# Kernel optimization log

Hardware: AMD Instinct MI355X
Metric: run time of the kernel (lower is better)

## Reference

```python
import jax, jax.numpy as jnp
import numpy as np

E = 21   # numParticipants (experts)
D = 128  # input features (hardcoded Linear(128,16))
H = 16   # hidden
N = 262144  # rows


def setup_inputs() -> dict:
    key = jax.random.key(0)
    ks = jax.random.split(key, 6)
    x = jax.random.normal(ks[0], (N, D), dtype=jnp.float32)
    sid = jax.random.randint(ks[1], (N,), 0, E)
    s1 = 1.0 / np.sqrt(D)
    W1 = jax.random.uniform(ks[2], (E, D, H), jnp.float32, -s1, s1)
    b1 = jax.random.uniform(ks[3], (E, H), jnp.float32, -s1, s1)
    s2 = 1.0 / np.sqrt(H)
    W2 = jax.random.uniform(ks[4], (E, H), jnp.float32, -s2, s2)  # Linear(16,1) weight, squeezed
    b2 = jax.random.uniform(ks[5], (E,), jnp.float32, -s2, s2)
    return {"x": x, "sid": sid, "W1": W1, "b1": b1, "W2": W2, "b2": b2}


def reference(x, sid, W1, b1, W2, b2):
    # Per-row expert MLP: h = relu(x @ W1[sid] + b1[sid]); y = relu(h . W2[sid] + b2[sid]).
    # Dropout(0.5) is identity in eval mode. Vectorized routing: compute first layer for
    # all 21 tiny experts ([N,E,H] ~ 350MB), then select the routed expert per row.
    h_all = jax.nn.relu(jnp.einsum('nd,edh->neh', x, W1) + b1[None, :, :])  # [N,E,H]
    h = jnp.take_along_axis(h_all, sid[:, None, None], axis=1)[:, 0, :]      # [N,H]
    y = jax.nn.relu(jnp.einsum('nh,nh->n', h, W2[sid]) + b2[sid])            # [N]
    return y[:, None]  # [N,1]
```

## Files before the change

kernel.cpp:

```cpp
#include <hip/hip_runtime.h>
#include <stdint.h>

#define N_ROWS 262144
#define DIM    128
#define HID    16
#define NEXP   21
#define NSEG   (N_ROWS / 64 + NEXP)
#define NBLK1  256
#define RPB    (N_ROWS / NBLK1)
#define RPT    (RPB / 256)

#define PADB     1040
#define WAVE_LDS (8 * PADB)
#define BLK_LDS  (4 * WAVE_LDS)

__global__ __launch_bounds__(256) void k_hist(const int* __restrict__ sid,
                                              int* __restrict__ counts,
                                              int* __restrict__ blockBase) {
    __shared__ int lh[NEXP];
    int t = threadIdx.x;
    if (t < NEXP) lh[t] = 0;
    __syncthreads();
    int base = blockIdx.x * RPB + t;
#pragma unroll
    for (int r = 0; r < RPT; r++) {
        atomicAdd(&lh[sid[base + r * 256]], 1);
    }
    __syncthreads();
    if (t < NEXP) blockBase[blockIdx.x * NEXP + t] = atomicAdd(&counts[t], lh[t]);
}

__global__ __launch_bounds__(256) void k_scatter(const int* __restrict__ sid,
                                                 const int* __restrict__ counts,
                                                 const int* __restrict__ blockBase,
                                                 int* __restrict__ buckets) {
    __shared__ int sbase[NEXP];
    __shared__ int lcur[NEXP];
    int t = threadIdx.x;
    if (t == 0) {
        int acc = 0;
        for (int e = 0; e < NEXP; e++) {
            sbase[e] = acc + blockBase[blockIdx.x * NEXP + e];
            acc += ((counts[e] + 63) >> 6) << 6;
        }
    }
    if (t < NEXP) lcur[t] = 0;
    __syncthreads();
    int base = blockIdx.x * RPB + t;
#pragma unroll
    for (int r = 0; r < RPT; r++) {
        int row = base + r * 256;
        int e = sid[row];
        int lp = atomicAdd(&lcur[e], 1);
        buckets[sbase[e] + lp] = row | (e << 24);
    }
}

typedef __attribute__((address_space(1))) const uint32_t gu32;
typedef __attribute__((address_space(3))) uint32_t lu32;

__device__ __forceinline__ void stage16(const float* gp, char* lp) {
    __builtin_amdgcn_global_load_lds((gu32*)(uintptr_t)gp,
                                     (lu32*)(uintptr_t)lp, 16, 0, 0);
}

__device__ __forceinline__ float bcast(float v, int lane) {
    return __uint_as_float(__builtin_amdgcn_readlane(__float_as_uint(v), lane));
}

__global__ __launch_bounds__(256, 4) void k_main4(const float* __restrict__ x,
                                                  const float* __restrict__ W1,
                                                  const float* __restrict__ b1,
                                                  const float* __restrict__ W2,
                                                  const float* __restrict__ b2,
                                                  const int* __restrict__ buckets,
                                                  float* __restrict__ out) {
    extern __shared__ char smem[];
    const int seg = blockIdx.x * 4 + (threadIdx.x >> 6);
    if (seg >= NSEG) return;
    const int lane = threadIdx.x & 63;
    char* waveLds = smem + (threadIdx.x >> 6) * WAVE_LDS;

    int ent = buckets[seg * 64 + lane];
    if (__ballot(ent >= 0) == 0ULL) return;
    const int e = __builtin_amdgcn_readfirstlane(ent) >> 24;
    const int row = ent & 0x00FFFFFF;
    const int vrow = (ent >= 0) ? row : 0;

    int rg[8];
#pragma unroll
    for (int g = 0; g < 8; g++) rg[g] = __shfl(vrow, g * 8 + (lane >> 3), 64);
    const int c8 = lane & 7;

    const float* __restrict__ w1 = W1 + e * (DIM * HID);
    float h[HID];
#pragma unroll
    for (int j = 0; j < HID; j++) h[j] = b1[e * HID + j];

    const char* rb = waveLds + (lane >> 3) * PADB + (lane & 7) * 128;

#pragma unroll 1
    for (int q = 0; q < 4; q++) {
        __builtin_amdgcn_s_waitcnt(0);
#pragma unroll
        for (int g = 0; g < 8; g++) {
            const float* gp = x + (size_t)rg[g] * DIM + q * 32 + c8 * 4;
            stage16(gp, waveLds + g * PADB + lane * 16);
        }
        const float* __restrict__ w1q = w1 + q * 512;
        float wq[8];
#pragma unroll
        for (int m = 0; m < 8; m++) wq[m] = w1q[m * 64 + lane];
        __builtin_amdgcn_s_waitcnt(0);
#pragma unroll
        for (int m = 0; m < 8; m++) {
            const float4 xv = *(const float4*)(rb + m * 16);
            const float xc[4] = {xv.x, xv.y, xv.z, xv.w};
#pragma unroll
            for (int c = 0; c < 4; c++) {
#pragma unroll
                for (int j = 0; j < HID; j++)
                    h[j] = fmaf(xc[c], bcast(wq[m], c * 16 + j), h[j]);
            }
        }
    }

    float acc = b2[e];
#pragma unroll
    for (int j = 0; j < HID; j++) acc = fmaf(fmaxf(h[j], 0.0f), W2[e * HID + j], acc);
    if (ent >= 0) out[row] = fmaxf(acc, 0.0f);
}

__global__ __launch_bounds__(256) void k_naive(const float* __restrict__ x,
                                               const int* __restrict__ sid,
                                               const float* __restrict__ W1,
                                               const float* __restrict__ b1,
                                               const float* __restrict__ W2,
                                               const float* __restrict__ b2,
                                               float* __restrict__ out) {
    int row = blockIdx.x * 256 + threadIdx.x;
    if (row >= N_ROWS) return;
    int e = sid[row];
    const float* w1 = W1 + e * (DIM * HID);
    const float* xr = x + (size_t)row * DIM;
    float h[HID];
#pragma unroll
    for (int j = 0; j < HID; j++) h[j] = b1[e * HID + j];
    for (int k = 0; k < DIM; k++) {
        float xk = xr[k];
#pragma unroll
        for (int j = 0; j < HID; j++) h[j] = fmaf(xk, w1[k * HID + j], h[j]);
    }
    float acc = b2[e];
#pragma unroll
    for (int j = 0; j < HID; j++) acc = fmaf(fmaxf(h[j], 0.0f), W2[e * HID + j], acc);
    out[row] = fmaxf(acc, 0.0f);
}

extern "C" void kernel_launch(void* const* d_in, const int* in_sizes, int n_in,
                              void* d_out, int out_size, void* d_ws, size_t ws_size,
                              hipStream_t stream) {
    const float* x   = (const float*)d_in[0];
    const int*   sid = (const int*)d_in[1];
    const float* W1  = (const float*)d_in[2];
    const float* b1  = (const float*)d_in[3];
    const float* W2  = (const float*)d_in[4];
    const float* b2  = (const float*)d_in[5];
    float* out = (float*)d_out;

    const size_t bucketBytes = (size_t)NSEG * 64 * sizeof(int);
    const size_t countBytes  = 32 * sizeof(int);
    const size_t bbBytes     = (size_t)NBLK1 * NEXP * sizeof(int);
    const size_t need = bucketBytes + countBytes + bbBytes;

    if (ws_size < need) {
        k_naive<<<(N_ROWS + 255) / 256, 256, 0, stream>>>(x, sid, W1, b1, W2, b2, out);
        return;
    }

    char* ws = (char*)d_ws;
    int* buckets   = (int*)ws;
    int* counts    = (int*)(ws + bucketBytes);
    int* blockBase = (int*)(ws + bucketBytes + countBytes);

    hipMemsetAsync(buckets, 0xFF, bucketBytes, stream);
    hipMemsetAsync(counts, 0, countBytes, stream);
    k_hist<<<NBLK1, 256, 0, stream>>>(sid, counts, blockBase);
    k_scatter<<<NBLK1, 256, 0, stream>>>(sid, counts, blockBase, buckets);
    k_main4<<<(NSEG + 3) / 4, 256, BLK_LDS, stream>>>(x, W1, b1, W2, b2, buckets, out);
}
```

Before: 220.9 us.

## Compute expert first layer with bf16x3 split MFMA instead of scalar FMAs

After: 220.9 us. Within noise of the previous version (-0.0%).

```diff
diff --git a/kernel.cpp b/kernel.cpp
--- a/kernel.cpp
+++ b/kernel.cpp
@@ -9,10 +9,6 @@
 #define NBLK1  256
 #define RPB    (N_ROWS / NBLK1)
 #define RPT    (RPB / 256)
-
-#define PADB     1040
-#define WAVE_LDS (8 * PADB)
-#define BLK_LDS  (4 * WAVE_LDS)
 
 __global__ __launch_bounds__(256) void k_hist(const int* __restrict__ sid,
                                               int* __restrict__ counts,
@@ -56,79 +52,97 @@
     }
 }
 
-typedef __attribute__((address_space(1))) const uint32_t gu32;
-typedef __attribute__((address_space(3))) uint32_t lu32;
-
-__device__ __forceinline__ void stage16(const float* gp, char* lp) {
-    __builtin_amdgcn_global_load_lds((gu32*)(uintptr_t)gp,
-                                     (lu32*)(uintptr_t)lp, 16, 0, 0);
-}
-
-__device__ __forceinline__ float bcast(float v, int lane) {
-    return __uint_as_float(__builtin_amdgcn_readlane(__float_as_uint(v), lane));
-}
-
-__global__ __launch_bounds__(256, 4) void k_main4(const float* __restrict__ x,
-                                                  const float* __restrict__ W1,
-                                                  const float* __restrict__ b1,
-                                                  const float* __restrict__ W2,
-                                                  const float* __restrict__ b2,
-                                                  const int* __restrict__ buckets,
-                                                  float* __restrict__ out) {
-    extern __shared__ char smem[];
+typedef __attribute__((ext_vector_type(8))) short bf16x8;
+typedef __attribute__((ext_vector_type(4))) float f32x4;
+
+__device__ __forceinline__ uint32_t pack2(uint32_t a, uint32_t b) {
+    return __builtin_amdgcn_perm(b, a, 0x07060302u);
+}
+
+__device__ __forceinline__ void cvt8(const float* f, bf16x8& fh, bf16x8& fl) {
+    union { uint32_t u[4]; bf16x8 v; } H, L;
+#pragma unroll
+    for (int i = 0; i < 4; i++) {
+        uint32_t a = __float_as_uint(f[2 * i]);
+        uint32_t b = __float_as_uint(f[2 * i + 1]);
+        H.u[i] = pack2(a, b);
+        float ra = f[2 * i]     - __uint_as_float(a & 0xffff0000u);
+        float rb = f[2 * i + 1] - __uint_as_float(b & 0xffff0000u);
+        L.u[i] = pack2(__float_as_uint(ra), __float_as_uint(rb));
+    }
+    fh = H.v; fl = L.v;
+}
+
+__global__ __launch_bounds__(256, 4) void k_mfma(const float* __restrict__ x,
+                                                 const float* __restrict__ W1,
+                                                 const float* __restrict__ b1,
+                                                 const float* __restrict__ W2,
+                                                 const float* __restrict__ b2,
+                                                 const int* __restrict__ buckets,
+                                                 float* __restrict__ out) {
     const int seg = blockIdx.x * 4 + (threadIdx.x >> 6);
     if (seg >= NSEG) return;
     const int lane = threadIdx.x & 63;
-    char* waveLds = smem + (threadIdx.x >> 6) * WAVE_LDS;
-
-    int ent = buckets[seg * 64 + lane];
+
+    const int ent = buckets[seg * 64 + lane];
     if (__ballot(ent >= 0) == 0ULL) return;
     const int e = __builtin_amdgcn_readfirstlane(ent) >> 24;
-    const int row = ent & 0x00FFFFFF;
-    const int vrow = (ent >= 0) ? row : 0;
-
-    int rg[8];
-#pragma unroll
-    for (int g = 0; g < 8; g++) rg[g] = __shfl(vrow, g * 8 + (lane >> 3), 64);
-    const int c8 = lane & 7;
+    const int row0 = __shfl(ent, 0, 64) & 0x00FFFFFF;
+    const int vrow = (ent >= 0) ? (ent & 0x00FFFFFF) : row0;
+
+    const int ncol  = lane & 15;
+    const int kbase = (lane >> 4) * 8;
+
+    int arow[4];
+#pragma unroll
+    for (int mt = 0; mt < 4; mt++) arow[mt] = __shfl(vrow, mt * 16 + ncol, 64);
 
     const float* __restrict__ w1 = W1 + e * (DIM * HID);
-    float h[HID];
-#pragma unroll
-    for (int j = 0; j < HID; j++) h[j] = b1[e * HID + j];
-
-    const char* rb = waveLds + (lane >> 3) * PADB + (lane & 7) * 128;
+    const float b1v = b1[e * HID + ncol];
+    const float w2v = W2[e * HID + ncol];
+    const float b2v = b2[e];
+
+    const f32x4 zero = {0.0f, 0.0f, 0.0f, 0.0f};
+    f32x4 acc[4] = {zero, zero, zero, zero};
 
 #pragma unroll 1
-    for (int q = 0; q < 4; q++) {
-        __builtin_amdgcn_s_waitcnt(0);
-#pragma unroll
-        for (int g = 0; g < 8; g++) {
-            const float* gp = x + (size_t)rg[g] * DIM + q * 32 + c8 * 4;
-            stage16(gp, waveLds + g * PADB + lane * 16);
+    for (int kt = 0; kt < 4; kt++) {
+        float bf[8];
+        const float* wp = w1 + (kt * 32 + kbase) * HID + ncol;
+#pragma unroll
+        for (int t = 0; t < 8; t++) bf[t] = wp[t * HID];
+        bf16x8 bh, bl;
+        cvt8(bf, bh, bl);
+
+#pragma unroll
+        for (int mt = 0; mt < 4; mt++) {
+            const float* xp = x + (size_t)arow[mt] * DIM + kt * 32 + kbase;
+            float af[8];
+            *(float4*)(af)     = *(const float4*)(xp);
+            *(float4*)(af + 4) = *(const float4*)(xp + 4);
+            bf16x8 ah, al;
+            cvt8(af, ah, al);
+            acc[mt] = __builtin_amdgcn_mfma_f32_16x16x32_bf16(ah, bh, acc[mt], 0, 0, 0);
+            acc[mt] = __builtin_amdgcn_mfma_f32_16x16x32_bf16(al, bh, acc[mt], 0, 0, 0);
+            acc[mt] = __builtin_amdgcn_mfma_f32_16x16x32_bf16(ah, bl, acc[mt], 0, 0, 0);
         }
-        const float* __restrict__ w1q = w1 + q * 512;
-        float wq[8];
-#pragma unroll
-        for (int m = 0; m < 8; m++) wq[m] = w1q[m * 64 + lane];
-        __builtin_amdgcn_s_waitcnt(0);
-#pragma unroll
-        for (int m = 0; m < 8; m++) {
-            const float4 xv = *(const float4*)(rb + m * 16);
-            const float xc[4] = {xv.x, xv.y, xv.z, xv.w};
-#pragma unroll
-            for (int c = 0; c < 4; c++) {
-#pragma unroll
-                for (int j = 0; j < HID; j++)
-                    h[j] = fmaf(xc[c], bcast(wq[m], c * 16 + j), h[j]);
-            }
+    }
+
+#pragma unroll
+    for (int mt = 0; mt < 4; mt++) {
+#pragma unroll
+        for (int r = 0; r < 4; r++) {
+            float c = fmaxf(acc[mt][r] + b1v, 0.0f) * w2v;
+            c += __shfl_xor(c, 1, 64);
+            c += __shfl_xor(c, 2, 64);
+            c += __shfl_xor(c, 4, 64);
+            c += __shfl_xor(c, 8, 64);
+            const int slot = mt * 16 + (lane >> 4) * 4 + r;
+            const int sent = __shfl(ent, slot, 64);
+            if (ncol == 0 && sent >= 0)
+                out[sent & 0x00FFFFFF] = fmaxf(c + b2v, 0.0f);
         }
     }
-
-    float acc = b2[e];
-#pragma unroll
-    for (int j = 0; j < HID; j++) acc = fmaf(fmaxf(h[j], 0.0f), W2[e * HID + j], acc);
-    if (ent >= 0) out[row] = fmaxf(acc, 0.0f);
 }
 
 __global__ __launch_bounds__(256) void k_naive(const float* __restrict__ x,
@@ -187,5 +201,5 @@
     hipMemsetAsync(counts, 0, countBytes, stream);
     k_hist<<<NBLK1, 256, 0, stream>>>(sid, counts, blockBase);
     k_scatter<<<NBLK1, 256, 0, stream>>>(sid, counts, blockBase, buckets);
-    k_main4<<<(NSEG + 3) / 4, 256, BLK_LDS, stream>>>(x, W1, b1, W2, b2, buckets, out);
-}
+    k_mfma<<<(NSEG + 3) / 4, 256, 0, stream>>>(x, W1, b1, W2, b2, buckets, out);
+}
```
